# Optimization experiments

Hardware: AMD Instinct MI355X
Metric: run time of the kernel (lower is better)

Reference implementation:

```python
import jax, jax.numpy as jnp
import numpy as np
from jax import lax

D_MODEL = 1024
BATCH = 4
SEQ = 4096
DECAY = 0.9
INPUT_SCALE = 0.1


def setup_inputs() -> dict:
    key = jax.random.key(0)
    k1, k2, k3 = jax.random.split(key, 3)
    scale_in = 1.0 / np.sqrt(D_MODEL)
    return {
        "x": jax.random.normal(k1, (BATCH, SEQ, D_MODEL), dtype=jnp.float32),
        "W_in": jax.random.normal(k2, (D_MODEL, 2 * D_MODEL), dtype=jnp.float32) * scale_in,
        "b_in": jnp.zeros((2 * D_MODEL,), dtype=jnp.float32),
        "W_out": jax.random.normal(k3, (D_MODEL, D_MODEL), dtype=jnp.float32) * scale_in,
        "b_out": jnp.zeros((D_MODEL,), dtype=jnp.float32),
    }


def reference(x, W_in, b_in, W_out, b_out):
    # x: [B, S, D]
    x_proj = jnp.einsum("bsd,de->bse", x, W_in) + b_in  # [B, S, 2D]
    x_gate, x_hidden = jnp.split(x_proj, 2, axis=-1)
    x_gated = jax.nn.sigmoid(x_gate) * jax.nn.silu(x_hidden)  # [B, S, D]

    # gated EMA scan: h_t = 0.9*h_{t-1} + 0.1*g_t, h_0 = 0
    def step(h, g_t):
        h = DECAY * h + INPUT_SCALE * g_t
        return h, h

    g_tm = jnp.swapaxes(x_gated, 0, 1)  # [S, B, D] time-major
    h0 = jnp.zeros((x.shape[0], x.shape[2]), dtype=x.dtype)
    _, hs = lax.scan(step, h0, g_tm)  # [S, B, D]
    hidden_seq = jnp.swapaxes(hs, 0, 1)  # [B, S, D]

    out = jnp.einsum("bsd,de->bse", hidden_seq, W_out) + b_out
    return out
```

## Files before the change

### kernel.cpp

```cpp
#include <hip/hip_runtime.h>
#include <hip/hip_bf16.h>

#define B_   4
#define S_   4096
#define D_   1024
#define M_   (B_ * S_)
#define K_   1024
#define BK   64
#define NT   (K_ / BK)

typedef __attribute__((ext_vector_type(4))) float f32x4;
typedef __attribute__((ext_vector_type(8))) short bf16x8;
typedef unsigned short ushort_t;
typedef unsigned int uint_t;

#define SCHEDB __builtin_amdgcn_sched_barrier(0)
#define MFMA16(a, b, c) __builtin_amdgcn_mfma_f32_16x16x32_bf16(a, b, c, 0, 0, 0)

__device__ inline ushort_t f2bf(float f) {
    union { float f; unsigned u; } v; v.f = f;
    unsigned r = v.u + 0x7fffu + ((v.u >> 16) & 1u);
    return (ushort_t)(r >> 16);
}
__device__ inline float bf2f(ushort_t s) {
    union { unsigned u; float f; } v; v.u = ((unsigned)s) << 16; return v.f;
}

__global__ __launch_bounds__(256) void prep_kernel(
    const float4* __restrict__ x, ushort_t* __restrict__ xb,
    const float* __restrict__ W_in, const float* __restrict__ W_out,
    ushort_t* __restrict__ winT, ushort_t* __restrict__ woT)
{
    const int bid = blockIdx.x, tid = threadIdx.x;
    if (bid < 8192) {
        int i = bid * 256 + tid;
        float4 a = x[2 * i], b = x[2 * i + 1];
        union { ushort_t s[8]; uint4 v; } u;
        u.s[0] = f2bf(a.x); u.s[1] = f2bf(a.y); u.s[2] = f2bf(a.z); u.s[3] = f2bf(a.w);
        u.s[4] = f2bf(b.x); u.s[5] = f2bf(b.y); u.s[6] = f2bf(b.z); u.s[7] = f2bf(b.w);
        ((uint4*)xb)[i] = u.v;
        return;
    }
    __shared__ float tile[32][33];
    const int tx = tid & 31, ty = tid >> 5;
    if (bid < 10240) {
        int wb = bid - 8192;
        int n0 = (wb & 63) * 32, k0 = (wb >> 6) * 32;
        int ci = (n0 >> 1) + (tx & 15) + ((tx & 16) ? 1024 : 0);
#pragma unroll
        for (int j = 0; j < 4; ++j)
            tile[ty + 8 * j][tx] = W_in[(long)(k0 + ty + 8 * j) * 2048 + ci];
        __syncthreads();
#pragma unroll
        for (int j = 0; j < 4; ++j)
            winT[(long)(n0 + ty + 8 * j) * 1024 + k0 + tx] = f2bf(tile[tx][ty + 8 * j]);
    } else {
        int wb = bid - 10240;
        int n0 = (wb & 31) * 32, k0 = (wb >> 5) * 32;
#pragma unroll
        for (int j = 0; j < 4; ++j)
            tile[ty + 8 * j][tx] = W_out[(long)(k0 + ty + 8 * j) * 1024 + n0 + tx];
        __syncthreads();
#pragma unroll
        for (int j = 0; j < 4; ++j)
            woT[(long)(n0 + ty + 8 * j) * 1024 + k0 + tx] = f2bf(tile[tx][ty + 8 * j]);
    }
}

__device__ inline void stage_half(const char* gtile, char* ldst, int soff0, int soff1, int w) {
    __builtin_amdgcn_global_load_lds((const __attribute__((address_space(1))) void*)(gtile + soff0),
                                     (__attribute__((address_space(3))) void*)(ldst + w * 2048), 16, 0, 0);
    __builtin_amdgcn_global_load_lds((const __attribute__((address_space(1))) void*)(gtile + soff1),
                                     (__attribute__((address_space(3))) void*)(ldst + w * 2048 + 1024), 16, 0, 0);
}

template<int NBN, int GATE>
__global__ __launch_bounds__(512, 1) void gemm8_kernel(
    const ushort_t* __restrict__ A, const ushort_t* __restrict__ Bm,
    const float* __restrict__ bias, void* __restrict__ outp)
{
    extern __shared__ char smem[];
    const int tid = threadIdx.x;
    const int l = tid & 63, w = tid >> 6;
    const int wm = w >> 2, wn = w & 3;
    const int lrow = l & 15, kgrp = l >> 4;

    const int nwg = gridDim.x, cpx = nwg >> 3, bid = blockIdx.x;
    const int wg = (bid & 7) * cpx + (bid >> 3);
    const long m0 = (long)(wg / NBN) * 256;
    const long n0 = (long)(wg % NBN) * 256;

    const char* gA = (const char*)A + m0 * 2048;
    const char* gB = (const char*)Bm + n0 * 2048;

    const int lsw = (((l & 7) ^ (l >> 3)) << 4);
    const int soff0 = ((w * 2 + 0) * 8 + (l >> 3)) * 2048 + lsw;
    const int soff1 = ((w * 2 + 1) * 8 + (l >> 3)) * 2048 + lsw;

    const int arow = (wm * 128 + lrow) * 128;
    const int brow = (wn * 64 + lrow) * 128;
    const int sw0 = ((kgrp ^ (l & 7)) << 4);
    const int sw1 = (((4 + kgrp) ^ (l & 7)) << 4);

    f32x4 acc[8][4];
#pragma unroll
    for (int i = 0; i < 8; ++i)
#pragma unroll
        for (int j = 0; j < 4; ++j) acc[i][j] = f32x4{0.f, 0.f, 0.f, 0.f};

    bf16x8 af[4][2], bf[2][2], af2[4][2], bf2[2][2];

    char* s1 = smem + 65536;
    stage_half(gA,              smem,          soff0, soff1, w);
    stage_half(gA + 262144,     smem + 16384,  soff0, soff1, w);
    stage_half(gB,              smem + 32768,  soff0, soff1, w);
    stage_half(gB + 262144,     smem + 49152,  soff0, soff1, w);
    stage_half(gA + 128,        s1,            soff0, soff1, w);
    stage_half(gA + 262144 + 128, s1 + 16384,  soff0, soff1, w);
    stage_half(gB + 128,        s1 + 32768,    soff0, soff1, w);
    stage_half(gB + 262144 + 128, s1 + 49152,  soff0, soff1, w);
    asm volatile("s_waitcnt vmcnt(8)" ::: "memory");
    __builtin_amdgcn_s_barrier();
#pragma unroll
    for (int fm = 0; fm < 4; ++fm) {
        af[fm][0] = *(const bf16x8*)(smem + arow + fm * 2048 + sw0);
        af[fm][1] = *(const bf16x8*)(smem + arow + fm * 2048 + sw1);
    }
#pragma unroll
    for (int fn = 0; fn < 2; ++fn) {
        bf[fn][0] = *(const bf16x8*)(smem + 32768 + brow + fn * 2048 + sw0);
        bf[fn][1] = *(const bf16x8*)(smem + 32768 + brow + fn * 2048 + sw1);
    }
    SCHEDB;

    for (int t = 0; t < NT; ++t) {
        char* cur = smem + ((t & 1) << 16);
        char* nxt = smem + (((t + 1) & 1) << 16);

#pragma unroll
        for (int fn = 0; fn < 2; ++fn) {
            bf2[fn][0] = *(const bf16x8*)(cur + 32768 + brow + (fn + 2) * 2048 + sw0);
            bf2[fn][1] = *(const bf16x8*)(cur + 32768 + brow + (fn + 2) * 2048 + sw1);
        }
        SCHEDB;
        asm volatile("s_waitcnt vmcnt(4)" ::: "memory");
        asm volatile("s_waitcnt lgkmcnt(4)" ::: "memory");
        SCHEDB;
        __builtin_amdgcn_s_setprio(1);
#pragma unroll
        for (int fm = 0; fm < 4; ++fm)
#pragma unroll
            for (int fn = 0; fn < 2; ++fn) {
                acc[fm][fn] = MFMA16(af[fm][0], bf[fn][0], acc[fm][fn]);
                acc[fm][fn] = MFMA16(af[fm][1], bf[fn][1], acc[fm][fn]);
            }
        __builtin_amdgcn_s_setprio(0);
        SCHEDB;
        __builtin_amdgcn_s_barrier();

#pragma unroll
        for (int fm = 0; fm < 4; ++fm) {
            af2[fm][0] = *(const bf16x8*)(cur + arow + (fm + 4) * 2048 + sw0);
            af2[fm][1] = *(const bf16x8*)(cur + arow + (fm + 4) * 2048 + sw1);
        }
        if (t + 2 < NT) stage_half(gA + (t + 2) * 128, cur, soff0, soff1, w);
        SCHEDB;
        asm volatile("s_waitcnt lgkmcnt(8)" ::: "memory");
        SCHEDB;
        __builtin_amdgcn_s_setprio(1);
#pragma unroll
        for (int fm = 0; fm < 4; ++fm)
#pragma unroll
            for (int fn = 0; fn < 2; ++fn) {
                acc[fm][fn + 2] = MFMA16(af[fm][0], bf2[fn][0], acc[fm][fn + 2]);
                acc[fm][fn + 2] = MFMA16(af[fm][1], bf2[fn][1], acc[fm][fn + 2]);
            }
        __builtin_amdgcn_s_setprio(0);
        SCHEDB;
        __builtin_amdgcn_s_barrier();

        if (t + 2 < NT) stage_half(gB + (t + 2) * 128, cur + 32768, soff0, soff1, w);
        SCHEDB;
        if (t < NT - 2) asm volatile("s_waitcnt vmcnt(6)" ::: "memory");
        else            asm volatile("s_waitcnt vmcnt(0)" ::: "memory");
        asm volatile("s_waitcnt lgkmcnt(0)" ::: "memory");
        SCHEDB;
        __builtin_amdgcn_s_setprio(1);
#pragma unroll
        for (int fm = 0; fm < 4; ++fm)
#pragma unroll
            for (int fn = 0; fn < 2; ++fn) {
                acc[fm + 4][fn] = MFMA16(af2[fm][0], bf[fn][0], acc[fm + 4][fn]);
                acc[fm + 4][fn] = MFMA16(af2[fm][1], bf[fn][1], acc[fm + 4][fn]);
            }
        __builtin_amdgcn_s_setprio(0);
        SCHEDB;
        __builtin_amdgcn_s_barrier();

        if (t + 1 < NT) {
#pragma unroll
            for (int fm = 0; fm < 4; ++fm) {
                af[fm][0] = *(const bf16x8*)(nxt + arow + fm * 2048 + sw0);
                af[fm][1] = *(const bf16x8*)(nxt + arow + fm * 2048 + sw1);
            }
#pragma unroll
            for (int fn = 0; fn < 2; ++fn) {
                bf[fn][0] = *(const bf16x8*)(nxt + 32768 + brow + fn * 2048 + sw0);
                bf[fn][1] = *(const bf16x8*)(nxt + 32768 + brow + fn * 2048 + sw1);
            }
        }
        if (t + 2 < NT) {
            stage_half(gB + 262144 + (t + 2) * 128, cur + 49152, soff0, soff1, w);
            stage_half(gA + 262144 + (t + 2) * 128, cur + 16384, soff0, soff1, w);
        }
        SCHEDB;
        __builtin_amdgcn_s_setprio(1);
#pragma unroll
        for (int fm = 0; fm < 4; ++fm)
#pragma unroll
            for (int fn = 0; fn < 2; ++fn) {
                acc[fm + 4][fn + 2] = MFMA16(af2[fm][0], bf2[fn][0], acc[fm + 4][fn + 2]);
                acc[fm + 4][fn + 2] = MFMA16(af2[fm][1], bf2[fn][1], acc[fm + 4][fn + 2]);
            }
        __builtin_amdgcn_s_setprio(0);
        SCHEDB;
        __builtin_amdgcn_s_barrier();
    }

    const long row0 = m0 + wm * 128 + kgrp * 4;
    if (GATE) {
        ushort_t* g = (ushort_t*)outp;
#pragma unroll
        for (int fm = 0; fm < 8; ++fm) {
#pragma unroll
            for (int fp = 0; fp < 2; ++fp) {
                int c = (int)(n0 >> 1) + wn * 32 + fp * 16 + lrow;
                float bg = bias[c], bh = bias[1024 + c];
#pragma unroll
                for (int r = 0; r < 4; ++r) {
                    long rr = row0 + fm * 16 + r;
                    float gate = acc[fm][fp * 2][r] + bg;
                    float hid  = acc[fm][fp * 2 + 1][r] + bh;
                    float sg = 1.0f / (1.0f + expf(-gate));
                    float sh = 1.0f / (1.0f + expf(-hid));
                    g[rr * 1024 + c] = f2bf(sg * hid * sh);
                }
            }
        }
    } else {
        float* o = (float*)outp;
#pragma unroll
        for (int fm = 0; fm < 8; ++fm)
#pragma unroll
            for (int fn = 0; fn < 4; ++fn) {
                int c = (int)n0 + wn * 64 + fn * 16 + lrow;
                float bo = bias[c];
#pragma unroll
                for (int r = 0; r < 4; ++r) {
                    long rr = row0 + fm * 16 + r;
                    o[rr * 1024 + c] = acc[fm][fn][r] + bo;
                }
            }
    }
}

__global__ void scan_kernel(const ushort_t* __restrict__ g, ushort_t* __restrict__ h) {
    int idx = blockIdx.x * 256 + threadIdx.x;
    int b = idx >> 9, d = (idx & 511) * 2;
    int chunk = blockIdx.y;
    const ushort_t* gb = g + (long)b * S_ * 1024 + d;
    ushort_t* hb = h + (long)b * S_ * 1024 + d;
    float h0 = 0.f, h1 = 0.f;
    int t0 = chunk * 128;
    int tw = t0 - 64; if (tw < 0) tw = 0;
#pragma unroll 4
    for (int t = tw; t < t0; ++t) {
        uint_t v = *(const uint_t*)(gb + (long)t * 1024);
        h0 = 0.9f * h0 + 0.1f * bf2f((ushort_t)(v & 0xffffu));
        h1 = 0.9f * h1 + 0.1f * bf2f((ushort_t)(v >> 16));
    }
#pragma unroll 4
    for (int t = t0; t < t0 + 128; ++t) {
        uint_t v = *(const uint_t*)(gb + (long)t * 1024);
        h0 = 0.9f * h0 + 0.1f * bf2f((ushort_t)(v & 0xffffu));
        h1 = 0.9f * h1 + 0.1f * bf2f((ushort_t)(v >> 16));
        *(uint_t*)(hb + (long)t * 1024) = (((uint_t)f2bf(h1)) << 16) | (uint_t)f2bf(h0);
    }
}

extern "C" void kernel_launch(void* const* d_in, const int* in_sizes, int n_in,
                              void* d_out, int out_size, void* d_ws, size_t ws_size,
                              hipStream_t stream) {
    const float* x     = (const float*)d_in[0];
    const float* W_in  = (const float*)d_in[1];
    const float* b_in  = (const float*)d_in[2];
    const float* W_out = (const float*)d_in[3];
    const float* b_out = (const float*)d_in[4];
    float* outp = (float*)d_out;

    char* ws = (char*)d_ws;
    ushort_t* xb   = (ushort_t*)ws;
    ushort_t* winT = (ushort_t*)(ws + 33554432);
    ushort_t* woT  = (ushort_t*)(ws + 33554432 + 4194304);
    ushort_t* gbuf = (ushort_t*)(ws + 33554432 + 6291456);

    hipFuncSetAttribute((const void*)&gemm8_kernel<8, 1>, hipFuncAttributeMaxDynamicSharedMemorySize, 131072);
    hipFuncSetAttribute((const void*)&gemm8_kernel<4, 0>, hipFuncAttributeMaxDynamicSharedMemorySize, 131072);

    prep_kernel<<<11264, 256, 0, stream>>>((const float4*)x, xb, W_in, W_out, winT, woT);
    gemm8_kernel<8, 1><<<512, 512, 131072, stream>>>(xb, winT, b_in, (void*)gbuf);
    scan_kernel<<<dim3(8, 32), 256, 0, stream>>>(gbuf, xb);
    gemm8_kernel<4, 0><<<256, 512, 131072, stream>>>(xb, woT, b_out, (void*)outp);
}
```

Before: 167.2 us.

## Switch GEMM inner loop from 16x16x32 to 32x32x16 bf16 MFMA tiles

Replaces the 16x16x32 MFMA instructions with 32x32x16 MFMA in both GEMM kernels. It reorganises the per-wave fragment loads, the accumulator layout and the epilogue indexing to match, and changes the W_in interleave in the prep kernel so gate and hidden columns fall into matching 32-wide blocks. The larger MFMA shape cuts the instruction count and the number of LDS fragment reads per FLOP. The cost is a different output-row mapping in the epilogue, which could give less coalesced stores, and a different register-pressure and scheduling profile within the existing waitcnt pattern.

```diff
diff --git a/kernel.cpp b/kernel.cpp
--- a/kernel.cpp
+++ b/kernel.cpp
@@ -10,12 +10,13 @@
 #define NT   (K_ / BK)
 
 typedef __attribute__((ext_vector_type(4))) float f32x4;
+typedef __attribute__((ext_vector_type(16))) float f32x16;
 typedef __attribute__((ext_vector_type(8))) short bf16x8;
 typedef unsigned short ushort_t;
 typedef unsigned int uint_t;
 
 #define SCHEDB __builtin_amdgcn_sched_barrier(0)
-#define MFMA16(a, b, c) __builtin_amdgcn_mfma_f32_16x16x32_bf16(a, b, c, 0, 0, 0)
+#define MFMA32(a, b, c) __builtin_amdgcn_mfma_f32_32x32x16_bf16(a, b, c, 0, 0, 0)
 
 __device__ inline ushort_t f2bf(float f) {
     union { float f; unsigned u; } v; v.f = f;
@@ -46,7 +47,7 @@
     if (bid < 10240) {
         int wb = bid - 8192;
         int n0 = (wb & 63) * 32, k0 = (wb >> 6) * 32;
-        int ci = (n0 >> 1) + (tx & 15) + ((tx & 16) ? 1024 : 0);
+        int ci = ((n0 >> 6) << 5) + tx + ((n0 & 32) ? 1024 : 0);
 #pragma unroll
         for (int j = 0; j < 4; ++j)
             tile[ty + 8 * j][tx] = W_in[(long)(k0 + ty + 8 * j) * 2048 + ci];
@@ -83,7 +84,7 @@
     const int tid = threadIdx.x;
     const int l = tid & 63, w = tid >> 6;
     const int wm = w >> 2, wn = w & 3;
-    const int lrow = l & 15, kgrp = l >> 4;
+    const int l31 = l & 31, lhi = l >> 5;
 
     const int nwg = gridDim.x, cpx = nwg >> 3, bid = blockIdx.x;
     const int wg = (bid & 7) * cpx + (bid >> 3);
@@ -97,18 +98,21 @@
     const int soff0 = ((w * 2 + 0) * 8 + (l >> 3)) * 2048 + lsw;
     const int soff1 = ((w * 2 + 1) * 8 + (l >> 3)) * 2048 + lsw;
 
-    const int arow = (wm * 128 + lrow) * 128;
-    const int brow = (wn * 64 + lrow) * 128;
-    const int sw0 = ((kgrp ^ (l & 7)) << 4);
-    const int sw1 = (((4 + kgrp) ^ (l & 7)) << 4);
-
-    f32x4 acc[8][4];
-#pragma unroll
-    for (int i = 0; i < 8; ++i)
-#pragma unroll
-        for (int j = 0; j < 4; ++j) acc[i][j] = f32x4{0.f, 0.f, 0.f, 0.f};
-
-    bf16x8 af[4][2], bf[2][2], af2[4][2], bf2[2][2];
+    const int arow = (wm * 128 + l31) * 128;
+    const int brow = 32768 + (wn * 64 + l31) * 128;
+    int swk[4];
+#pragma unroll
+    for (int ks = 0; ks < 4; ++ks) swk[ks] = (((ks * 2 + lhi) ^ (l & 7)) << 4);
+
+    f32x16 acc[4][2];
+#pragma unroll
+    for (int i = 0; i < 4; ++i)
+#pragma unroll
+        for (int j = 0; j < 2; ++j)
+#pragma unroll
+            for (int p = 0; p < 16; ++p) acc[i][j][p] = 0.f;
+
+    bf16x8 af[2][4], bf[4], af2[2][4], bf2[4];
 
     char* s1 = smem + 65536;
     stage_half(gA,              smem,          soff0, soff1, w);
@@ -122,15 +126,13 @@
     asm volatile("s_waitcnt vmcnt(8)" ::: "memory");
     __builtin_amdgcn_s_barrier();
 #pragma unroll
-    for (int fm = 0; fm < 4; ++fm) {
-        af[fm][0] = *(const bf16x8*)(smem + arow + fm * 2048 + sw0);
-        af[fm][1] = *(const bf16x8*)(smem + arow + fm * 2048 + sw1);
-    }
-#pragma unroll
-    for (int fn = 0; fn < 2; ++fn) {
-        bf[fn][0] = *(const bf16x8*)(smem + 32768 + brow + fn * 2048 + sw0);
-        bf[fn][1] = *(const bf16x8*)(smem + 32768 + brow + fn * 2048 + sw1);
-    }
+    for (int fm = 0; fm < 2; ++fm)
+#pragma unroll
+        for (int ks = 0; ks < 4; ++ks)
+            af[fm][ks] = *(const bf16x8*)(smem + arow + fm * 4096 + swk[ks]);
+#pragma unroll
+    for (int ks = 0; ks < 4; ++ks)
+        bf[ks] = *(const bf16x8*)(smem + brow + swk[ks]);
     SCHEDB;
 
     for (int t = 0; t < NT; ++t) {
@@ -138,43 +140,37 @@
         char* nxt = smem + (((t + 1) & 1) << 16);
 
 #pragma unroll
-        for (int fn = 0; fn < 2; ++fn) {
-            bf2[fn][0] = *(const bf16x8*)(cur + 32768 + brow + (fn + 2) * 2048 + sw0);
-            bf2[fn][1] = *(const bf16x8*)(cur + 32768 + brow + (fn + 2) * 2048 + sw1);
-        }
+        for (int ks = 0; ks < 4; ++ks)
+            bf2[ks] = *(const bf16x8*)(cur + brow + 4096 + swk[ks]);
         SCHEDB;
         asm volatile("s_waitcnt vmcnt(4)" ::: "memory");
         asm volatile("s_waitcnt lgkmcnt(4)" ::: "memory");
         SCHEDB;
         __builtin_amdgcn_s_setprio(1);
 #pragma unroll
-        for (int fm = 0; fm < 4; ++fm)
-#pragma unroll
-            for (int fn = 0; fn < 2; ++fn) {
-                acc[fm][fn] = MFMA16(af[fm][0], bf[fn][0], acc[fm][fn]);
-                acc[fm][fn] = MFMA16(af[fm][1], bf[fn][1], acc[fm][fn]);
-            }
+        for (int ks = 0; ks < 4; ++ks)
+#pragma unroll
+            for (int fm = 0; fm < 2; ++fm)
+                acc[fm][0] = MFMA32(af[fm][ks], bf[ks], acc[fm][0]);
         __builtin_amdgcn_s_setprio(0);
         SCHEDB;
         __builtin_amdgcn_s_barrier();
 
 #pragma unroll
-        for (int fm = 0; fm < 4; ++fm) {
-            af2[fm][0] = *(const bf16x8*)(cur + arow + (fm + 4) * 2048 + sw0);
-            af2[fm][1] = *(const bf16x8*)(cur + arow + (fm + 4) * 2048 + sw1);
-        }
+        for (int fm = 0; fm < 2; ++fm)
+#pragma unroll
+            for (int ks = 0; ks < 4; ++ks)
+                af2[fm][ks] = *(const bf16x8*)(cur + arow + (fm + 2) * 4096 + swk[ks]);
         if (t + 2 < NT) stage_half(gA + (t + 2) * 128, cur, soff0, soff1, w);
         SCHEDB;
         asm volatile("s_waitcnt lgkmcnt(8)" ::: "memory");
         SCHEDB;
         __builtin_amdgcn_s_setprio(1);
 #pragma unroll
-        for (int fm = 0; fm < 4; ++fm)
-#pragma unroll
-            for (int fn = 0; fn < 2; ++fn) {
-                acc[fm][fn + 2] = MFMA16(af[fm][0], bf2[fn][0], acc[fm][fn + 2]);
-                acc[fm][fn + 2] = MFMA16(af[fm][1], bf2[fn][1], acc[fm][fn + 2]);
-            }
+        for (int ks = 0; ks < 4; ++ks)
+#pragma unroll
+            for (int fm = 0; fm < 2; ++fm)
+                acc[fm][1] = MFMA32(af[fm][ks], bf2[ks], acc[fm][1]);
         __builtin_amdgcn_s_setprio(0);
         SCHEDB;
         __builtin_amdgcn_s_barrier();
@@ -187,27 +183,23 @@
         SCHEDB;
         __builtin_amdgcn_s_setprio(1);
 #pragma unroll
-        for (int fm = 0; fm < 4; ++fm)
-#pragma unroll
-            for (int fn = 0; fn < 2; ++fn) {
-                acc[fm + 4][fn] = MFMA16(af2[fm][0], bf[fn][0], acc[fm + 4][fn]);
-                acc[fm + 4][fn] = MFMA16(af2[fm][1], bf[fn][1], acc[fm + 4][fn]);
-            }
+        for (int ks = 0; ks < 4; ++ks)
+#pragma unroll
+            for (int fm = 0; fm < 2; ++fm)
+                acc[fm + 2][0] = MFMA32(af2[fm][ks], bf[ks], acc[fm + 2][0]);
         __builtin_amdgcn_s_setprio(0);
         SCHEDB;
         __builtin_amdgcn_s_barrier();
 
         if (t + 1 < NT) {
 #pragma unroll
-            for (int fm = 0; fm < 4; ++fm) {
-                af[fm][0] = *(const bf16x8*)(nxt + arow + fm * 2048 + sw0);
-                af[fm][1] = *(const bf16x8*)(nxt + arow + fm * 2048 + sw1);
-            }
-#pragma unroll
-            for (int fn = 0; fn < 2; ++fn) {
-                bf[fn][0] = *(const bf16x8*)(nxt + 32768 + brow + fn * 2048 + sw0);
-                bf[fn][1] = *(const bf16x8*)(nxt + 32768 + brow + fn * 2048 + sw1);
-            }
+            for (int fm = 0; fm < 2; ++fm)
+#pragma unroll
+                for (int ks = 0; ks < 4; ++ks)
+                    af[fm][ks] = *(const bf16x8*)(nxt + arow + fm * 4096 + swk[ks]);
+#pragma unroll
+            for (int ks = 0; ks < 4; ++ks)
+                bf[ks] = *(const bf16x8*)(nxt + brow + swk[ks]);
         }
         if (t + 2 < NT) {
             stage_half(gB + 262144 + (t + 2) * 128, cur + 49152, soff0, soff1, w);
@@ -216,51 +208,45 @@
         SCHEDB;
         __builtin_amdgcn_s_setprio(1);
 #pragma unroll
-        for (int fm = 0; fm < 4; ++fm)
-#pragma unroll
-            for (int fn = 0; fn < 2; ++fn) {
-                acc[fm + 4][fn + 2] = MFMA16(af2[fm][0], bf2[fn][0], acc[fm + 4][fn + 2]);
-                acc[fm + 4][fn + 2] = MFMA16(af2[fm][1], bf2[fn][1], acc[fm + 4][fn + 2]);
-            }
+        for (int ks = 0; ks < 4; ++ks)
+#pragma unroll
+            for (int fm = 0; fm < 2; ++fm)
+                acc[fm + 2][1] = MFMA32(af2[fm][ks], bf2[ks], acc[fm + 2][1]);
         __builtin_amdgcn_s_setprio(0);
         SCHEDB;
         __builtin_amdgcn_s_barrier();
     }
 
-    const long row0 = m0 + wm * 128 + kgrp * 4;
+    const long rbase = m0 + wm * 128 + 4 * lhi;
     if (GATE) {
         ushort_t* g = (ushort_t*)outp;
-#pragma unroll
-        for (int fm = 0; fm < 8; ++fm) {
-#pragma unroll
-            for (int fp = 0; fp < 2; ++fp) {
-                int c = (int)(n0 >> 1) + wn * 32 + fp * 16 + lrow;
-                float bg = bias[c], bh = bias[1024 + c];
-#pragma unroll
-                for (int r = 0; r < 4; ++r) {
-                    long rr = row0 + fm * 16 + r;
-                    float gate = acc[fm][fp * 2][r] + bg;
-                    float hid  = acc[fm][fp * 2 + 1][r] + bh;
-                    float sg = 1.0f / (1.0f + expf(-gate));
-                    float sh = 1.0f / (1.0f + expf(-hid));
-                    g[rr * 1024 + c] = f2bf(sg * hid * sh);
-                }
+        const int c = (int)(n0 >> 1) + wn * 32 + l31;
+        const float bg = bias[c], bh = bias[1024 + c];
+#pragma unroll
+        for (int fm = 0; fm < 4; ++fm)
+#pragma unroll
+            for (int p = 0; p < 16; ++p) {
+                long rr = rbase + fm * 32 + (p & 3) + 8 * (p >> 2);
+                float gate = acc[fm][0][p] + bg;
+                float hid  = acc[fm][1][p] + bh;
+                float sg = 1.0f / (1.0f + expf(-gate));
+                float sh = 1.0f / (1.0f + expf(-hid));
+                g[rr * 1024 + c] = f2bf(sg * hid * sh);
             }
-        }
     } else {
         float* o = (float*)outp;
 #pragma unroll
-        for (int fm = 0; fm < 8; ++fm)
-#pragma unroll
-            for (int fn = 0; fn < 4; ++fn) {
-                int c = (int)n0 + wn * 64 + fn * 16 + lrow;
-                float bo = bias[c];
-#pragma unroll
-                for (int r = 0; r < 4; ++r) {
-                    long rr = row0 + fm * 16 + r;
-                    o[rr * 1024 + c] = acc[fm][fn][r] + bo;
+        for (int fn = 0; fn < 2; ++fn) {
+            int c = (int)n0 + wn * 64 + fn * 32 + l31;
+            float bo = bias[c];
+#pragma unroll
+            for (int fm = 0; fm < 4; ++fm)
+#pragma unroll
+                for (int p = 0; p < 16; ++p) {
+                    long rr = rbase + fm * 32 + (p & 3) + 8 * (p >> 2);
+                    o[rr * 1024 + c] = acc[fm][fn][p] + bo;
                 }
-            }
+        }
     }
 }
 
```

Result: slower. 189.2 us (+13.2%).
